# Kernel optimization log

Hardware: AMD Instinct MI355X
Metric: run time of the kernel (lower is better)

## Reference

```python
import jax, jax.numpy as jnp
import numpy as np

C_IN = 128      # pair channel
C_HID = 32      # per-head hidden dim
H = 4           # heads
INF = 1e9
LN_EPS = 1e-5


def setup_inputs() -> dict:
    key = jax.random.key(0)
    ks = jax.random.split(key, 8)
    B, N = 1, 256
    s = 0.02
    return {
        "x": jax.random.normal(ks[0], (B, N, N, C_IN), dtype=jnp.float32),
        "mask": jnp.ones((B, N, N), dtype=jnp.float32),
        "ln_w": jnp.ones((C_IN,), dtype=jnp.float32),
        "ln_b": jnp.zeros((C_IN,), dtype=jnp.float32),
        "w_b": jax.random.normal(ks[1], (H, C_IN), dtype=jnp.float32) * s,      # triangle-bias linear (no bias)
        "w_q": jax.random.normal(ks[2], (H * C_HID, C_IN), dtype=jnp.float32) * s,
        "w_k": jax.random.normal(ks[3], (H * C_HID, C_IN), dtype=jnp.float32) * s,
        "w_v": jax.random.normal(ks[4], (H * C_HID, C_IN), dtype=jnp.float32) * s,
        "w_g": jax.random.normal(ks[5], (H * C_HID, C_IN), dtype=jnp.float32) * s,
        "b_g": jnp.ones((H * C_HID,), dtype=jnp.float32),
        "w_o": jax.random.normal(ks[6], (C_IN, H * C_HID), dtype=jnp.float32) * s,
        "b_o": jnp.zeros((C_IN,), dtype=jnp.float32),
    }


def reference(x, mask, ln_w, ln_b, w_b, w_q, w_k, w_v, w_g, b_g, w_o, b_o):
    # starting=True -> no transpose
    # LayerNorm over channel dim
    mu = jnp.mean(x, axis=-1, keepdims=True)
    var = jnp.var(x, axis=-1, keepdims=True)
    xn = (x - mu) * jax.lax.rsqrt(var + LN_EPS) * ln_w + ln_b            # [B,I,J,C]

    # mask bias: [B, I, 1, 1, J]
    mask_bias = (INF * (mask - 1.0))[..., :, None, None, :]

    # triangle bias: linear -> [B,I,J,H] -> permute -> [B,H,I,J] -> [B,1,H,I,J]
    tri_bias = jnp.einsum("bijc,hc->bhij", xn, w_b)[:, None]

    # QKV projections, per-head: weights reshaped to [H, D, C]
    Wq = w_q.reshape(H, C_HID, C_IN)
    Wk = w_k.reshape(H, C_HID, C_IN)
    Wv = w_v.reshape(H, C_HID, C_IN)
    scale = 1.0 / np.sqrt(C_HID)
    q = jnp.einsum("bijc,hdc->bihjd", xn, Wq) * scale                    # [B,I,H,J,D]
    k = jnp.einsum("bijc,hdc->bihjd", xn, Wk)
    v = jnp.einsum("bijc,hdc->bihjd", xn, Wv)

    # attention over the J (column) axis of each row i
    a = jnp.einsum("bihqd,bihkd->bihqk", q, k) + mask_bias + tri_bias    # [B,I,H,J,J]
    a = jax.nn.softmax(a, axis=-1)
    o = jnp.einsum("bihqk,bihkd->biqhd", a, v)                           # [B,I,J,H,D]

    # sigmoid gating
    g = jax.nn.sigmoid(jnp.einsum("bijc,ec->bije", xn, w_g) + b_g)       # [B,I,J,H*D]
    o = o.reshape(*o.shape[:-2], H * C_HID) * g

    # output projection
    return jnp.einsum("bije,ce->bijc", o, w_o) + b_o                     # [B,I,J,C_in]
```

## Files before the change

kernel.cpp:

```cpp
#include <hip/hip_runtime.h>

#define N 256
#define C 128
#define H 4
#define D 32
#define NP (N*N)
#define LN_EPS 1e-5f
#define LOG2E 1.4426950408889634f

__device__ __forceinline__ void barrier_lgkm() {
    __asm__ volatile("s_waitcnt lgkmcnt(0)" ::: "memory");
    __builtin_amdgcn_sched_barrier(0);
    __builtin_amdgcn_s_barrier();
    __builtin_amdgcn_sched_barrier(0);
}

using f32x4 = __attribute__((ext_vector_type(4))) float;
using bf8   = __attribute__((ext_vector_type(8))) short;
using u16x4 = __attribute__((ext_vector_type(4))) unsigned short;

__device__ __forceinline__ float bf2f(ushort u) {
    union { uint u; float f; } v; v.u = ((uint)u) << 16; return v.f;
}
__device__ __forceinline__ ushort f2bf(float f) {
    union { float f; uint u; } v; v.f = f;
    uint u = v.u;
    u += 0x7fffu + ((u >> 16) & 1u);
    return (ushort)(u >> 16);
}
__device__ __forceinline__ ushort f2bf_trunc(float f) {
    union { float f; uint u; } v; v.f = f;
    return (ushort)(v.u >> 16);
}

__global__ __launch_bounds__(256) void prep_weights(
    const float* __restrict__ wq, const float* __restrict__ wk,
    const float* __restrict__ wv, const float* __restrict__ wg,
    const float* __restrict__ wb, const float* __restrict__ wo,
    ushort* __restrict__ Wcat, ushort* __restrict__ WbPad, ushort* __restrict__ Wo)
{
    int t = blockIdx.x * 256 + threadIdx.x;
    const float scale = 0.17677669529663689f * LOG2E;
    float v;
    if (t < 16384)       v = wq[t] * scale;
    else if (t < 32768)  v = wk[t - 16384];
    else if (t < 49152)  v = wv[t - 32768];
    else                 v = wg[t - 49152];
    Wcat[t] = f2bf(v);
    if (t < 16384) Wo[t] = f2bf(wo[t]);
    if (t < 2048)  WbPad[t] = (t < 512) ? f2bf(wb[t]) : (ushort)0;
}

__global__ __launch_bounds__(512, 4) void ln_proj(
    const float* __restrict__ x, const float* __restrict__ lnw,
    const float* __restrict__ lnb, const ushort* __restrict__ Wcat,
    const ushort* __restrict__ WbPad, const float* __restrict__ bg,
    ushort* __restrict__ qb, ushort* __restrict__ kb,
    ushort* __restrict__ vbT, ushort* __restrict__ gate,
    ushort* __restrict__ tri_p)
{
    __shared__ ushort At[64 * 128];
    int mt = blockIdx.x;
    int t  = threadIdx.x;
    int wave = t >> 6, lane = t & 63;
    int lane32 = lane & 31, rsel = lane >> 5;

    {
        const float4 w4 = ((const float4*)lnw)[lane32];
        const float4 b4 = ((const float4*)lnb)[lane32];
        const float* xb = x + (size_t)mt * 64 * C;
        float4 xv[4];
        #pragma unroll
        for (int pp = 0; pp < 4; pp++) {
            int r = pp * 16 + wave * 2 + rsel;
            xv[pp] = ((const float4*)(xb + r * C))[lane32];
        }
        #pragma unroll
        for (int pp = 0; pp < 4; pp++) {
            int r = pp * 16 + wave * 2 + rsel;
            float4 v = xv[pp];
            float s  = v.x + v.y + v.z + v.w;
            float ss = v.x*v.x + v.y*v.y + v.z*v.z + v.w*v.w;
            #pragma unroll
            for (int m = 1; m < 32; m <<= 1) {
                s  += __shfl_xor(s, m, 64);
                ss += __shfl_xor(ss, m, 64);
            }
            float mean = s * (1.f / 128.f);
            float var  = ss * (1.f / 128.f) - mean * mean;
            float rstd = rsqrtf(var + LN_EPS);
            u16x4 o;
            o[0] = f2bf((v.x - mean) * rstd * w4.x + b4.x);
            o[1] = f2bf((v.y - mean) * rstd * w4.y + b4.y);
            o[2] = f2bf((v.z - mean) * rstd * w4.z + b4.z);
            o[3] = f2bf((v.w - mean) * rstd * w4.w + b4.w);
            int c8 = lane32 >> 1;
            int chunk = r * 16 + (c8 ^ (r & 7));
            *(u16x4*)&At[chunk * 8 + (lane32 & 1) * 4] = o;
        }
    }
    barrier_lgkm();

    int lrow = lane & 15, quad = lane >> 4;
    int wr = wave >> 2, wc = wave & 3;

    bf8 afr[4][2];
    #pragma unroll
    for (int ks = 0; ks < 4; ks++) {
        int c8 = ks * 4 + quad;
        #pragma unroll
        for (int mi = 0; mi < 2; mi++) {
            int row = wr * 32 + mi * 16 + lrow;
            afr[ks][mi] = *(const bf8*)&At[(row * 16 + (c8 ^ (row & 7))) * 8];
        }
    }

    if (wc == 0) {
        f32x4 at0 = (f32x4){0.f,0.f,0.f,0.f}, at1 = (f32x4){0.f,0.f,0.f,0.f};
        #pragma unroll
        for (int ks = 0; ks < 4; ks++) {
            bf8 bt = *(const bf8*)(WbPad + lrow * C + (ks * 4 + quad) * 8);
            at0 = __builtin_amdgcn_mfma_f32_16x16x32_bf16(afr[ks][0], bt, at0, 0, 0, 0);
            at1 = __builtin_amdgcn_mfma_f32_16x16x32_bf16(afr[ks][1], bt, at1, 0, 0, 0);
        }
        if (lrow < 4) {
            int q = mt >> 2;
            int qc = q >> 4, quadq = (q >> 2) & 3, rr = q & 3;
            #pragma unroll
            for (int mi = 0; mi < 2; mi++) {
                #pragma unroll
                for (int r = 0; r < 4; r++) {
                    int k = (mt & 3) * 64 + wr * 32 + mi * 16 + quad * 4 + r;
                    int n = k >> 4, lk = k & 15;
                    int lanet = quadq * 16 + lk;
                    int v2 = n * 4 + rr, j = v2 >> 3, m2 = v2 & 7;
                    float val = (mi == 0) ? at0[r] : at1[r];
                    tri_p[lrow * 65536 + ((qc * 8 + j) * 64 + lanet) * 8 + m2] =
                        f2bf(val * LOG2E);
                }
            }
        }
    }

    #pragma unroll 1
    for (int nt = 0; nt < 4; nt++) {
        const ushort* Wt = Wcat + (size_t)nt * 128 * C;
        f32x4 acc[2][2];
        #pragma unroll
        for (int mi = 0; mi < 2; mi++)
            #pragma unroll
            for (int ni = 0; ni < 2; ni++) acc[mi][ni] = (f32x4){0.f, 0.f, 0.f, 0.f};

        #pragma unroll
        for (int ks = 0; ks < 4; ks++) {
            int c8 = ks * 4 + quad;
            bf8 b0 = *(const bf8*)(Wt + (size_t)(wc * 32 + lrow)      * C + c8 * 8);
            bf8 b1 = *(const bf8*)(Wt + (size_t)(wc * 32 + 16 + lrow) * C + c8 * 8);
            acc[0][0] = __builtin_amdgcn_mfma_f32_16x16x32_bf16(afr[ks][0], b0, acc[0][0], 0, 0, 0);
            acc[0][1] = __builtin_amdgcn_mfma_f32_16x16x32_bf16(afr[ks][0], b1, acc[0][1], 0, 0, 0);
            acc[1][0] = __builtin_amdgcn_mfma_f32_16x16x32_bf16(afr[ks][1], b0, acc[1][0], 0, 0, 0);
            acc[1][1] = __builtin_amdgcn_mfma_f32_16x16x32_bf16(afr[ks][1], b1, acc[1][1], 0, 0, 0);
        }

        barrier_lgkm();
        if (nt == 2) {
            #pragma unroll
            for (int mi = 0; mi < 2; mi++) {
                #pragma unroll
                for (int ni = 0; ni < 2; ni++) {
                    int col = wc * 32 + ni * 16 + lrow;
                    #pragma unroll
                    for (int r = 0; r < 4; r++) {
                        int keyl = wr * 32 + mi * 16 + quad * 4 + r;
                        At[col * 64 + (keyl ^ ((col & 7) << 3))] = f2bf(acc[mi][ni][r]);
                    }
                }
            }
            barrier_lgkm();
            int i_row = mt >> 2, kq = mt & 3;
            #pragma unroll
            for (int itr = 0; itr < 2; itr++) {
                int oidx = itr * 512 + t;
                int col = oidx >> 3, kc = oidx & 7;
                bf8 val = *(const bf8*)&At[col * 64 + ((kc * 8) ^ ((col & 7) << 3))];
                *(bf8*)&vbT[(size_t)(i_row * 128 + col) * N + kq * 64 + kc * 8] = val;
            }
        } else {
            ushort* dst = (nt == 0) ? qb : (nt == 1) ? kb : gate;
            float g0 = 0.f, g1 = 0.f;
            if (nt == 3) { g0 = bg[wc * 32 + lrow]; g1 = bg[wc * 32 + 16 + lrow]; }
            #pragma unroll
            for (int mi = 0; mi < 2; mi++) {
                #pragma unroll
                for (int ni = 0; ni < 2; ni++) {
                    int col = wc * 32 + ni * 16 + lrow;
                    #pragma unroll
                    for (int r = 0; r < 4; r++) {
                        int row = wr * 32 + mi * 16 + quad * 4 + r;
                        float vv = acc[mi][ni][r];
                        if (nt == 3)
                            vv = 1.f / (1.f + __expf(-(vv + ((ni == 0) ? g0 : g1))));
                        At[(row * 16 + ((col >> 3) ^ (row & 7))) * 8 + (col & 7)] = f2bf(vv);
                    }
                }
            }
            barrier_lgkm();
            #pragma unroll
            for (int itr = 0; itr < 2; itr++) {
                int oidx = itr * 512 + t;
                int row = oidx >> 4, c8 = oidx & 15;
                bf8 val = *(const bf8*)&At[(row * 16 + (c8 ^ (row & 7))) * 8];
                *(bf8*)&dst[(size_t)(mt * 64 + row) * C + c8 * 8] = val;
            }
        }
    }
}

__global__ __launch_bounds__(512, 4) void attn_out(
    const ushort* __restrict__ qb, const ushort* __restrict__ kb,
    const ushort* __restrict__ vbT, const ushort* __restrict__ tri_p,
    const float* __restrict__ mask, const ushort* __restrict__ gate,
    const ushort* __restrict__ Wo, const float* __restrict__ bo,
    float* __restrict__ out)
{
    __shared__ ushort Kf[8192];
    __shared__ ushort Vf[8192];
    __shared__ ushort Pf[8][2048];

    int i  = blockIdx.x;
    int qh = blockIdx.y;
    int t  = threadIdx.x;
    int wave = t >> 6, lane = t & 63;
    int lrow = lane & 15, quad = lane >> 4;
    int qc = qh * 8 + wave;

    float mb[16];
    #pragma unroll
    for (int n = 0; n < 16; n++)
        mb[n] = (1e9f * LOG2E) * (mask[i * N + n * 16 + lrow] - 1.0f);

    f32x4 oacc[8];
    #pragma unroll
    for (int ct = 0; ct < 8; ct++) oacc[ct] = (f32x4){0.f, 0.f, 0.f, 0.f};

    ushort* Pw = &Pf[wave][0];
    const int pq = quad * 32 + (lrow & 7);
    const int l3 = (lrow >> 3) & 1;

    #pragma unroll 1
    for (int h = 0; h < 4; h++) {
        bf8 aq = *(const bf8*)(qb + (size_t)(i * N + qc * 16 + lrow) * C
                               + h * D + quad * 8);
        barrier_lgkm();
        {
            const ushort* kt = kb + (size_t)(i * N) * C + h * D;
            #pragma unroll
            for (int it = 0; it < 2; it++) {
                int idx = it * 512 + t;
                int key = idx >> 2, d0 = (idx & 3) * 8;
                bf8 kv = *(const bf8*)(kt + (size_t)key * C + d0);
                int c = (idx >> 6) * 64 + (idx & 3) * 16 + ((idx >> 2) & 15);
                *(bf8*)&Kf[c * 8] = kv;
            }
        }
        {
            const ushort* vt = vbT + (size_t)((i * H + h) * D) * N;
            #pragma unroll
            for (int it = 0; it < 2; it++) {
                int idx = it * 512 + t;
                bf8 vv = *(const bf8*)(vt + idx * 8);
                int c = (idx >> 9) * 512 + ((idx >> 2) & 7) * 64 + (idx & 3) * 16 + ((idx >> 5) & 15);
                c ^= (c >> 6) & 7;
                *(bf8*)&Vf[c * 8] = vv;
            }
        }
        barrier_lgkm();

        float sum[4] = {0.f, 0.f, 0.f, 0.f};
        f32x4 o[2];
        o[0] = (f32x4){0.f, 0.f, 0.f, 0.f};
        o[1] = (f32x4){0.f, 0.f, 0.f, 0.f};
        const ushort* trih = tri_p + (size_t)h * 65536;

        #pragma unroll
        for (int half = 0; half < 2; half++) {
            const ushort* tp = trih + ((size_t)(qc * 8 + half * 4) * 64 + lane) * 8;
            #pragma unroll
            for (int p = 0; p < 4; p++) {
                bf8 tf = *(const bf8*)(tp + p * 512);
                #pragma unroll
                for (int j = 0; j < 2; j++) {
                    int n8 = p * 2 + j;
                    bf8 kf = *(const bf8*)&Kf[((half * 8 + n8) * 64 + lane) * 8];
                    f32x4 s = __builtin_amdgcn_mfma_f32_16x16x32_bf16(
                        aq, kf, (f32x4){0.f, 0.f, 0.f, 0.f}, 0, 0, 0);
                    int pa = (n8 >> 1) * 512 + (((n8 << 1) + l3) & 3) * 128 + pq;
                    #pragma unroll
                    for (int r = 0; r < 4; r++) {
                        float tb = bf2f(((const ushort*)&tf)[j * 4 + r]);
                        float e  = exp2f(s[r] + tb + mb[half * 8 + n8]);
                        sum[r]  += e;
                        Pw[pa + r * 8] = f2bf_trunc(e);
                    }
                }
            }
            __asm__ volatile("s_waitcnt lgkmcnt(0)" ::: "memory");
            __builtin_amdgcn_sched_barrier(0);

            __builtin_amdgcn_s_setprio(1);
            #pragma unroll
            for (int ks = 0; ks < 4; ks++) {
                bf8 ap = *(const bf8*)&Pw[(ks * 64 + lane) * 8];
                int ksg = half * 4 + ks;
                #pragma unroll
                for (int nv = 0; nv < 2; nv++) {
                    int c = nv * 512 + ksg * 64 + (lane ^ (ksg & 7));
                    bf8 bv = *(const bf8*)&Vf[c * 8];
                    o[nv] = __builtin_amdgcn_mfma_f32_16x16x32_bf16(ap, bv, o[nv], 0, 0, 0);
                }
            }
            __builtin_amdgcn_s_setprio(0);
        }

        #pragma unroll
        for (int r = 0; r < 4; r++) {
            float s = sum[r];
            s += __shfl_xor(s, 1, 64);
            s += __shfl_xor(s, 2, 64);
            s += __shfl_xor(s, 4, 64);
            s += __shfl_xor(s, 8, 64);
            sum[r] = 1.f / s;
        }
        const ushort* gt = gate + (size_t)(i * N + qc * 16) * C + h * D;
        #pragma unroll
        for (int nv = 0; nv < 2; nv++) {
            #pragma unroll
            for (int r = 0; r < 4; r++) {
                float g = bf2f(gt[(quad * 4 + r) * C + nv * 16 + lrow]);
                float val = o[nv][r] * sum[r] * g;
                Pw[(nv * 2 + l3) * 128 + pq + r * 8] = f2bf(val);
            }
        }
        __asm__ volatile("s_waitcnt lgkmcnt(0)" ::: "memory");
        __builtin_amdgcn_sched_barrier(0);

        bf8 ap = *(const bf8*)&Pw[lane * 8];
        __builtin_amdgcn_s_setprio(1);
        #pragma unroll
        for (int ct = 0; ct < 8; ct++) {
            bf8 wv = *(const bf8*)(Wo + (size_t)(ct * 16 + lrow) * 128 + h * D + quad * 8);
            oacc[ct] = __builtin_amdgcn_mfma_f32_16x16x32_bf16(ap, wv, oacc[ct], 0, 0, 0);
        }
        __builtin_amdgcn_s_setprio(0);
    }

    #pragma unroll
    for (int ct = 0; ct < 8; ct++) {
        float bias = bo[ct * 16 + lrow];
        #pragma unroll
        for (int r = 0; r < 4; r++) {
            int qg = qc * 16 + quad * 4 + r;
            out[(size_t)(i * N + qg) * C + ct * 16 + lrow] = oacc[ct][r] + bias;
        }
    }
}

extern "C" void kernel_launch(void* const* d_in, const int* in_sizes, int n_in,
                              void* d_out, int out_size, void* d_ws, size_t ws_size,
                              hipStream_t stream)
{
    const float* x    = (const float*)d_in[0];
    const float* mask = (const float*)d_in[1];
    const float* lnw  = (const float*)d_in[2];
    const float* lnb  = (const float*)d_in[3];
    const float* wb   = (const float*)d_in[4];
    const float* wq   = (const float*)d_in[5];
    const float* wk   = (const float*)d_in[6];
    const float* wv   = (const float*)d_in[7];
    const float* wg   = (const float*)d_in[8];
    const float* bg   = (const float*)d_in[9];
    const float* wo   = (const float*)d_in[10];
    const float* bo   = (const float*)d_in[11];
    float* out = (float*)d_out;

    uintptr_t w = (uintptr_t)d_ws;
    ushort* qb    = (ushort*)w; w += (size_t)NP * C * 2;
    ushort* kb    = (ushort*)w; w += (size_t)NP * C * 2;
    ushort* vbT   = (ushort*)w; w += (size_t)NP * C * 2;
    ushort* gate  = (ushort*)w; w += (size_t)NP * C * 2;
    ushort* tri_p = (ushort*)w; w += (size_t)H * NP * 2;
    ushort* Wcat  = (ushort*)w; w += 512 * 128 * 2;
    ushort* WbPad = (ushort*)w; w += 16 * 128 * 2;
    ushort* Wo    = (ushort*)w; w += 128 * 128 * 2;

    prep_weights<<<256, 256, 0, stream>>>(wq, wk, wv, wg, wb, wo, Wcat, WbPad, Wo);
    ln_proj<<<NP / 64, 512, 0, stream>>>(x, lnw, lnb, Wcat, WbPad, bg,
                                         qb, kb, vbT, gate, tri_p);
    attn_out<<<dim3(N, 2), 512, 0, stream>>>(qb, kb, vbT, tri_p, mask, gate,
                                             Wo, bo, out);
}
```

Baseline: 184.4 us.

## Fuse LN, QKVG projection and row attention into one per-row kernel

The q/k/v/gate projection now runs inside the attention kernel, one 1024-thread block per row i. LayerNorm output stays in LDS and K/V are built directly in shared memory, so the large bf16 q/k/vT/gate intermediates no longer round-trip through global memory. The triangle bias moves to a separate lightweight kernel that recomputes LayerNorm and does a scalar dot-product reduction, and the mask bias is staged in LDS. In exchange, x is read and normalised twice, LDS use per block is much larger, and there are only 256 blocks, which may limit occupancy and latency hiding.

New measurement: 227.6 us. 1.23x slower.

```diff
diff --git a/kernel.cpp b/kernel.cpp
--- a/kernel.cpp
+++ b/kernel.cpp
@@ -14,6 +14,10 @@
     __builtin_amdgcn_s_barrier();
     __builtin_amdgcn_sched_barrier(0);
 }
+__device__ __forceinline__ void drain_lds() {
+    __asm__ volatile("s_waitcnt lgkmcnt(0)" ::: "memory");
+    __builtin_amdgcn_sched_barrier(0);
+}
 
 using f32x4 = __attribute__((ext_vector_type(4))) float;
 using bf8   = __attribute__((ext_vector_type(8))) short;
@@ -36,8 +40,8 @@
 __global__ __launch_bounds__(256) void prep_weights(
     const float* __restrict__ wq, const float* __restrict__ wk,
     const float* __restrict__ wv, const float* __restrict__ wg,
-    const float* __restrict__ wb, const float* __restrict__ wo,
-    ushort* __restrict__ Wcat, ushort* __restrict__ WbPad, ushort* __restrict__ Wo)
+    const float* __restrict__ wo,
+    ushort* __restrict__ Wcat, ushort* __restrict__ Wo)
 {
     int t = blockIdx.x * 256 + threadIdx.x;
     const float scale = 0.17677669529663689f * LOG2E;
@@ -48,37 +52,94 @@
     else                 v = wg[t - 49152];
     Wcat[t] = f2bf(v);
     if (t < 16384) Wo[t] = f2bf(wo[t]);
-    if (t < 2048)  WbPad[t] = (t < 512) ? f2bf(wb[t]) : (ushort)0;
-}
-
-__global__ __launch_bounds__(512, 4) void ln_proj(
+}
+
+__global__ __launch_bounds__(256) void ln_tri(
+    const float* __restrict__ x, const float* __restrict__ lnw,
+    const float* __restrict__ lnb, const float* __restrict__ wb,
+    ushort* __restrict__ tri_p)
+{
+    int t = threadIdx.x;
+    int wave = t >> 6, lane = t & 63;
+    int lane32 = lane & 31, rsel = lane >> 5;
+    const float4 w4 = ((const float4*)lnw)[lane32];
+    const float4 b4 = ((const float4*)lnb)[lane32];
+    float4 wb0 = ((const float4*)(wb      ))[lane32];
+    float4 wb1 = ((const float4*)(wb + 128))[lane32];
+    float4 wb2 = ((const float4*)(wb + 256))[lane32];
+    float4 wb3 = ((const float4*)(wb + 384))[lane32];
+
+    #pragma unroll 1
+    for (int pp = 0; pp < 8; pp++) {
+        int p = blockIdx.x * 64 + pp * 8 + wave * 2 + rsel;
+        float4 v = ((const float4*)(x + (size_t)p * C))[lane32];
+        float s  = v.x + v.y + v.z + v.w;
+        float ss = v.x*v.x + v.y*v.y + v.z*v.z + v.w*v.w;
+        #pragma unroll
+        for (int m = 1; m < 32; m <<= 1) {
+            s  += __shfl_xor(s, m, 64);
+            ss += __shfl_xor(ss, m, 64);
+        }
+        float mean = s * (1.f / 128.f);
+        float var  = ss * (1.f / 128.f) - mean * mean;
+        float rstd = rsqrtf(var + LN_EPS);
+        float x0 = (v.x - mean) * rstd * w4.x + b4.x;
+        float x1 = (v.y - mean) * rstd * w4.y + b4.y;
+        float x2 = (v.z - mean) * rstd * w4.z + b4.z;
+        float x3 = (v.w - mean) * rstd * w4.w + b4.w;
+        float a0 = x0*wb0.x + x1*wb0.y + x2*wb0.z + x3*wb0.w;
+        float a1 = x0*wb1.x + x1*wb1.y + x2*wb1.z + x3*wb1.w;
+        float a2 = x0*wb2.x + x1*wb2.y + x2*wb2.z + x3*wb2.w;
+        float a3 = x0*wb3.x + x1*wb3.y + x2*wb3.z + x3*wb3.w;
+        #pragma unroll
+        for (int m = 1; m < 32; m <<= 1) {
+            a0 += __shfl_xor(a0, m, 64);
+            a1 += __shfl_xor(a1, m, 64);
+            a2 += __shfl_xor(a2, m, 64);
+            a3 += __shfl_xor(a3, m, 64);
+        }
+        if (lane32 < 4) {
+            float av = (lane32 == 0) ? a0 : (lane32 == 1) ? a1
+                     : (lane32 == 2) ? a2 : a3;
+            int q = p >> 8, k = p & 255;
+            int qc = q >> 4, quadq = (q >> 2) & 3, rr = q & 3;
+            int n = k >> 4, lk = k & 15;
+            int lanet = quadq * 16 + lk;
+            int v2 = n * 4 + rr, j = v2 >> 3, m2 = v2 & 7;
+            tri_p[lane32 * 65536 + ((qc * 8 + j) * 64 + lanet) * 8 + m2] =
+                f2bf(av * LOG2E);
+        }
+    }
+}
+
+__global__ __launch_bounds__(1024, 4) void row_fused(
     const float* __restrict__ x, const float* __restrict__ lnw,
     const float* __restrict__ lnb, const ushort* __restrict__ Wcat,
-    const ushort* __restrict__ WbPad, const float* __restrict__ bg,
-    ushort* __restrict__ qb, ushort* __restrict__ kb,
-    ushort* __restrict__ vbT, ushort* __restrict__ gate,
-    ushort* __restrict__ tri_p)
+    const float* __restrict__ bg, const ushort* __restrict__ tri_p,
+    const float* __restrict__ mask, const ushort* __restrict__ Wo,
+    const float* __restrict__ bo, float* __restrict__ out)
 {
-    __shared__ ushort At[64 * 128];
-    int mt = blockIdx.x;
-    int t  = threadIdx.x;
+    __shared__ ushort Xn[256 * 128];
+    __shared__ ushort Kf[8192];
+    __shared__ ushort Vf[8192];
+    __shared__ ushort Pf[16 * 1024];
+    __shared__ float  Ml[256];
+
+    int i = blockIdx.x;
+    int t = threadIdx.x;
     int wave = t >> 6, lane = t & 63;
     int lane32 = lane & 31, rsel = lane >> 5;
+    int lrow = lane & 15, quad = lane >> 4;
 
     {
         const float4 w4 = ((const float4*)lnw)[lane32];
         const float4 b4 = ((const float4*)lnb)[lane32];
-        const float* xb = x + (size_t)mt * 64 * C;
-        float4 xv[4];
-        #pragma unroll
-        for (int pp = 0; pp < 4; pp++) {
-            int r = pp * 16 + wave * 2 + rsel;
-            xv[pp] = ((const float4*)(xb + r * C))[lane32];
-        }
-        #pragma unroll
-        for (int pp = 0; pp < 4; pp++) {
-            int r = pp * 16 + wave * 2 + rsel;
-            float4 v = xv[pp];
+        const float* xb = x + (size_t)i * N * C;
+        if (t < 256) Ml[t] = (1e9f * LOG2E) * (mask[i * N + t] - 1.f);
+        #pragma unroll
+        for (int pp = 0; pp < 8; pp++) {
+            int r = pp * 32 + wave * 2 + rsel;
+            float4 v = ((const float4*)(xb + r * C))[lane32];
             float s  = v.x + v.y + v.z + v.w;
             float ss = v.x*v.x + v.y*v.y + v.z*v.z + v.w*v.w;
             #pragma unroll
@@ -96,232 +157,126 @@
             o[3] = f2bf((v.w - mean) * rstd * w4.w + b4.w);
             int c8 = lane32 >> 1;
             int chunk = r * 16 + (c8 ^ (r & 7));
-            *(u16x4*)&At[chunk * 8 + (lane32 & 1) * 4] = o;
+            *(u16x4*)&Xn[chunk * 8 + (lane32 & 1) * 4] = o;
         }
     }
     barrier_lgkm();
-
-    int lrow = lane & 15, quad = lane >> 4;
-    int wr = wave >> 2, wc = wave & 3;
-
-    bf8 afr[4][2];
-    #pragma unroll
-    for (int ks = 0; ks < 4; ks++) {
-        int c8 = ks * 4 + quad;
-        #pragma unroll
-        for (int mi = 0; mi < 2; mi++) {
-            int row = wr * 32 + mi * 16 + lrow;
-            afr[ks][mi] = *(const bf8*)&At[(row * 16 + (c8 ^ (row & 7))) * 8];
-        }
-    }
-
-    if (wc == 0) {
-        f32x4 at0 = (f32x4){0.f,0.f,0.f,0.f}, at1 = (f32x4){0.f,0.f,0.f,0.f};
-        #pragma unroll
-        for (int ks = 0; ks < 4; ks++) {
-            bf8 bt = *(const bf8*)(WbPad + lrow * C + (ks * 4 + quad) * 8);
-            at0 = __builtin_amdgcn_mfma_f32_16x16x32_bf16(afr[ks][0], bt, at0, 0, 0, 0);
-            at1 = __builtin_amdgcn_mfma_f32_16x16x32_bf16(afr[ks][1], bt, at1, 0, 0, 0);
-        }
-        if (lrow < 4) {
-            int q = mt >> 2;
-            int qc = q >> 4, quadq = (q >> 2) & 3, rr = q & 3;
-            #pragma unroll
-            for (int mi = 0; mi < 2; mi++) {
-                #pragma unroll
-                for (int r = 0; r < 4; r++) {
-                    int k = (mt & 3) * 64 + wr * 32 + mi * 16 + quad * 4 + r;
-                    int n = k >> 4, lk = k & 15;
-                    int lanet = quadq * 16 + lk;
-                    int v2 = n * 4 + rr, j = v2 >> 3, m2 = v2 & 7;
-                    float val = (mi == 0) ? at0[r] : at1[r];
-                    tri_p[lrow * 65536 + ((qc * 8 + j) * 64 + lanet) * 8 + m2] =
-                        f2bf(val * LOG2E);
-                }
-            }
-        }
-    }
-
-    #pragma unroll 1
-    for (int nt = 0; nt < 4; nt++) {
-        const ushort* Wt = Wcat + (size_t)nt * 128 * C;
-        f32x4 acc[2][2];
-        #pragma unroll
-        for (int mi = 0; mi < 2; mi++)
-            #pragma unroll
-            for (int ni = 0; ni < 2; ni++) acc[mi][ni] = (f32x4){0.f, 0.f, 0.f, 0.f};
-
-        #pragma unroll
-        for (int ks = 0; ks < 4; ks++) {
-            int c8 = ks * 4 + quad;
-            bf8 b0 = *(const bf8*)(Wt + (size_t)(wc * 32 + lrow)      * C + c8 * 8);
-            bf8 b1 = *(const bf8*)(Wt + (size_t)(wc * 32 + 16 + lrow) * C + c8 * 8);
-            acc[0][0] = __builtin_amdgcn_mfma_f32_16x16x32_bf16(afr[ks][0], b0, acc[0][0], 0, 0, 0);
-            acc[0][1] = __builtin_amdgcn_mfma_f32_16x16x32_bf16(afr[ks][0], b1, acc[0][1], 0, 0, 0);
-            acc[1][0] = __builtin_amdgcn_mfma_f32_16x16x32_bf16(afr[ks][1], b0, acc[1][0], 0, 0, 0);
-            acc[1][1] = __builtin_amdgcn_mfma_f32_16x16x32_bf16(afr[ks][1], b1, acc[1][1], 0, 0, 0);
-        }
-
-        barrier_lgkm();
-        if (nt == 2) {
-            #pragma unroll
-            for (int mi = 0; mi < 2; mi++) {
-                #pragma unroll
-                for (int ni = 0; ni < 2; ni++) {
-                    int col = wc * 32 + ni * 16 + lrow;
-                    #pragma unroll
-                    for (int r = 0; r < 4; r++) {
-                        int keyl = wr * 32 + mi * 16 + quad * 4 + r;
-                        At[col * 64 + (keyl ^ ((col & 7) << 3))] = f2bf(acc[mi][ni][r]);
-                    }
-                }
-            }
-            barrier_lgkm();
-            int i_row = mt >> 2, kq = mt & 3;
-            #pragma unroll
-            for (int itr = 0; itr < 2; itr++) {
-                int oidx = itr * 512 + t;
-                int col = oidx >> 3, kc = oidx & 7;
-                bf8 val = *(const bf8*)&At[col * 64 + ((kc * 8) ^ ((col & 7) << 3))];
-                *(bf8*)&vbT[(size_t)(i_row * 128 + col) * N + kq * 64 + kc * 8] = val;
-            }
-        } else {
-            ushort* dst = (nt == 0) ? qb : (nt == 1) ? kb : gate;
-            float g0 = 0.f, g1 = 0.f;
-            if (nt == 3) { g0 = bg[wc * 32 + lrow]; g1 = bg[wc * 32 + 16 + lrow]; }
-            #pragma unroll
-            for (int mi = 0; mi < 2; mi++) {
-                #pragma unroll
-                for (int ni = 0; ni < 2; ni++) {
-                    int col = wc * 32 + ni * 16 + lrow;
-                    #pragma unroll
-                    for (int r = 0; r < 4; r++) {
-                        int row = wr * 32 + mi * 16 + quad * 4 + r;
-                        float vv = acc[mi][ni][r];
-                        if (nt == 3)
-                            vv = 1.f / (1.f + __expf(-(vv + ((ni == 0) ? g0 : g1))));
-                        At[(row * 16 + ((col >> 3) ^ (row & 7))) * 8 + (col & 7)] = f2bf(vv);
-                    }
-                }
-            }
-            barrier_lgkm();
-            #pragma unroll
-            for (int itr = 0; itr < 2; itr++) {
-                int oidx = itr * 512 + t;
-                int row = oidx >> 4, c8 = oidx & 15;
-                bf8 val = *(const bf8*)&At[(row * 16 + (c8 ^ (row & 7))) * 8];
-                *(bf8*)&dst[(size_t)(mt * 64 + row) * C + c8 * 8] = val;
-            }
-        }
-    }
-}
-
-__global__ __launch_bounds__(512, 4) void attn_out(
-    const ushort* __restrict__ qb, const ushort* __restrict__ kb,
-    const ushort* __restrict__ vbT, const ushort* __restrict__ tri_p,
-    const float* __restrict__ mask, const ushort* __restrict__ gate,
-    const ushort* __restrict__ Wo, const float* __restrict__ bo,
-    float* __restrict__ out)
-{
-    __shared__ ushort Kf[8192];
-    __shared__ ushort Vf[8192];
-    __shared__ ushort Pf[8][2048];
-
-    int i  = blockIdx.x;
-    int qh = blockIdx.y;
-    int t  = threadIdx.x;
-    int wave = t >> 6, lane = t & 63;
-    int lrow = lane & 15, quad = lane >> 4;
-    int qc = qh * 8 + wave;
-
-    float mb[16];
-    #pragma unroll
-    for (int n = 0; n < 16; n++)
-        mb[n] = (1e9f * LOG2E) * (mask[i * N + n * 16 + lrow] - 1.0f);
 
     f32x4 oacc[8];
     #pragma unroll
     for (int ct = 0; ct < 8; ct++) oacc[ct] = (f32x4){0.f, 0.f, 0.f, 0.f};
 
-    ushort* Pw = &Pf[wave][0];
+    ushort* Pw = Pf + wave * 1024;
     const int pq = quad * 32 + (lrow & 7);
     const int l3 = (lrow >> 3) & 1;
 
     #pragma unroll 1
     for (int h = 0; h < 4; h++) {
-        bf8 aq = *(const bf8*)(qb + (size_t)(i * N + qc * 16 + lrow) * C
-                               + h * D + quad * 8);
+        bf8 afr[4];
+        #pragma unroll
+        for (int ks = 0; ks < 4; ks++) {
+            int row = wave * 16 + lrow;
+            afr[ks] = *(const bf8*)&Xn[(row * 16 + ((ks * 4 + quad) ^ (row & 7))) * 8];
+        }
+        f32x4 qa[2], ka[2], va[2], ga[2];
+        #pragma unroll
+        for (int ni = 0; ni < 2; ni++) {
+            qa[ni] = (f32x4){0.f,0.f,0.f,0.f}; ka[ni] = (f32x4){0.f,0.f,0.f,0.f};
+            va[ni] = (f32x4){0.f,0.f,0.f,0.f}; ga[ni] = (f32x4){0.f,0.f,0.f,0.f};
+        }
+        const ushort* Wq_ = Wcat + (size_t)(h * 32) * C;
+        const ushort* Wk_ = Wcat + (size_t)(128 + h * 32) * C;
+        const ushort* Wv_ = Wcat + (size_t)(256 + h * 32) * C;
+        const ushort* Wg_ = Wcat + (size_t)(384 + h * 32) * C;
+        #pragma unroll
+        for (int ks = 0; ks < 4; ks++) {
+            #pragma unroll
+            for (int ni = 0; ni < 2; ni++) {
+                size_t ro = (size_t)(ni * 16 + lrow) * C + (ks * 4 + quad) * 8;
+                qa[ni] = __builtin_amdgcn_mfma_f32_16x16x32_bf16(afr[ks], *(const bf8*)(Wq_ + ro), qa[ni], 0, 0, 0);
+                ka[ni] = __builtin_amdgcn_mfma_f32_16x16x32_bf16(afr[ks], *(const bf8*)(Wk_ + ro), ka[ni], 0, 0, 0);
+                va[ni] = __builtin_amdgcn_mfma_f32_16x16x32_bf16(afr[ks], *(const bf8*)(Wv_ + ro), va[ni], 0, 0, 0);
+                ga[ni] = __builtin_amdgcn_mfma_f32_16x16x32_bf16(afr[ks], *(const bf8*)(Wg_ + ro), ga[ni], 0, 0, 0);
+            }
+        }
         barrier_lgkm();
+
+        #pragma unroll
+        for (int ni = 0; ni < 2; ni++) {
+            int d = lrow + 16 * ni;
+            #pragma unroll
+            for (int r = 0; r < 4; r++) {
+                int key = wave * 16 + quad * 4 + r;
+                Kf[((key >> 4) * 64 + (d >> 3) * 16 + (key & 15)) * 8 + (d & 7)] =
+                    f2bf(ka[ni][r]);
+                Vf[((d >> 4) * 512 + (key >> 5) * 64 +
+                    ((((key >> 3) & 3) * 16 + (d & 15)) ^ ((key >> 5) & 7))) * 8 +
+                   (key & 7)] = f2bf(va[ni][r]);
+                Pw[((d >> 3) * 16 + quad * 4 + r) * 8 + (d & 7)] = f2bf(qa[ni][r]);
+            }
+        }
+        float gr[2][4];
         {
-            const ushort* kt = kb + (size_t)(i * N) * C + h * D;
-            #pragma unroll
-            for (int it = 0; it < 2; it++) {
-                int idx = it * 512 + t;
-                int key = idx >> 2, d0 = (idx & 3) * 8;
-                bf8 kv = *(const bf8*)(kt + (size_t)key * C + d0);
-                int c = (idx >> 6) * 64 + (idx & 3) * 16 + ((idx >> 2) & 15);
-                *(bf8*)&Kf[c * 8] = kv;
-            }
-        }
-        {
-            const ushort* vt = vbT + (size_t)((i * H + h) * D) * N;
-            #pragma unroll
-            for (int it = 0; it < 2; it++) {
-                int idx = it * 512 + t;
-                bf8 vv = *(const bf8*)(vt + idx * 8);
-                int c = (idx >> 9) * 512 + ((idx >> 2) & 7) * 64 + (idx & 3) * 16 + ((idx >> 5) & 15);
-                c ^= (c >> 6) & 7;
-                *(bf8*)&Vf[c * 8] = vv;
-            }
+            float gb0 = bg[h * 32 + lrow], gb1 = bg[h * 32 + 16 + lrow];
+            #pragma unroll
+            for (int ni = 0; ni < 2; ni++)
+                #pragma unroll
+                for (int r = 0; r < 4; r++)
+                    gr[ni][r] = 1.f / (1.f + __expf(-(ga[ni][r] + (ni ? gb1 : gb0))));
         }
         barrier_lgkm();
+        bf8 aq = *(const bf8*)&Pw[(quad * 16 + lrow) * 8];
 
         float sum[4] = {0.f, 0.f, 0.f, 0.f};
-        f32x4 o[2];
-        o[0] = (f32x4){0.f, 0.f, 0.f, 0.f};
-        o[1] = (f32x4){0.f, 0.f, 0.f, 0.f};
+        f32x4 o2[2];
+        o2[0] = (f32x4){0.f,0.f,0.f,0.f};
+        o2[1] = (f32x4){0.f,0.f,0.f,0.f};
         const ushort* trih = tri_p + (size_t)h * 65536;
 
         #pragma unroll
         for (int half = 0; half < 2; half++) {
-            const ushort* tp = trih + ((size_t)(qc * 8 + half * 4) * 64 + lane) * 8;
-            #pragma unroll
-            for (int p = 0; p < 4; p++) {
-                bf8 tf = *(const bf8*)(tp + p * 512);
+            const ushort* tp = trih + ((size_t)(wave * 8 + half * 4) * 64 + lane) * 8;
+            bf8 tf[4];
+            #pragma unroll
+            for (int jj = 0; jj < 4; jj++)
+                tf[jj] = *(const bf8*)(tp + jj * 512);
+            float mbh[8];
+            #pragma unroll
+            for (int j8 = 0; j8 < 8; j8++)
+                mbh[j8] = Ml[(half * 8 + j8) * 16 + lrow];
+
+            #pragma unroll
+            for (int qq = 0; qq < 2; qq++) {
                 #pragma unroll
-                for (int j = 0; j < 2; j++) {
-                    int n8 = p * 2 + j;
-                    bf8 kf = *(const bf8*)&Kf[((half * 8 + n8) * 64 + lane) * 8];
+                for (int j = 0; j < 4; j++) {
+                    int n8h = qq * 4 + j;
+                    bf8 kf = *(const bf8*)&Kf[((half * 8 + n8h) * 64 + lane) * 8];
                     f32x4 s = __builtin_amdgcn_mfma_f32_16x16x32_bf16(
-                        aq, kf, (f32x4){0.f, 0.f, 0.f, 0.f}, 0, 0, 0);
-                    int pa = (n8 >> 1) * 512 + (((n8 << 1) + l3) & 3) * 128 + pq;
+                        aq, kf, (f32x4){0.f,0.f,0.f,0.f}, 0, 0, 0);
+                    int pa = (j >> 1) * 512 + (((j << 1) + l3) & 3) * 128 + pq;
                     #pragma unroll
                     for (int r = 0; r < 4; r++) {
-                        float tb = bf2f(((const ushort*)&tf)[j * 4 + r]);
-                        float e  = exp2f(s[r] + tb + mb[half * 8 + n8]);
+                        float tb = bf2f(((const ushort*)&tf[n8h >> 1])[((n8h & 1) << 2) + r]);
+                        float e  = exp2f(s[r] + tb + mbh[n8h]);
                         sum[r]  += e;
                         Pw[pa + r * 8] = f2bf_trunc(e);
                     }
                 }
-            }
-            __asm__ volatile("s_waitcnt lgkmcnt(0)" ::: "memory");
-            __builtin_amdgcn_sched_barrier(0);
-
-            __builtin_amdgcn_s_setprio(1);
-            #pragma unroll
-            for (int ks = 0; ks < 4; ks++) {
-                bf8 ap = *(const bf8*)&Pw[(ks * 64 + lane) * 8];
-                int ksg = half * 4 + ks;
+                drain_lds();
+                __builtin_amdgcn_s_setprio(1);
                 #pragma unroll
-                for (int nv = 0; nv < 2; nv++) {
-                    int c = nv * 512 + ksg * 64 + (lane ^ (ksg & 7));
-                    bf8 bv = *(const bf8*)&Vf[c * 8];
-                    o[nv] = __builtin_amdgcn_mfma_f32_16x16x32_bf16(ap, bv, o[nv], 0, 0, 0);
+                for (int ksl = 0; ksl < 2; ksl++) {
+                    bf8 ap = *(const bf8*)&Pw[(ksl * 64 + lane) * 8];
+                    int ksg = half * 4 + qq * 2 + ksl;
+                    #pragma unroll
+                    for (int nv = 0; nv < 2; nv++) {
+                        bf8 bv = *(const bf8*)&Vf[(nv * 512 + ksg * 64 + (lane ^ (ksg & 7))) * 8];
+                        o2[nv] = __builtin_amdgcn_mfma_f32_16x16x32_bf16(ap, bv, o2[nv], 0, 0, 0);
+                    }
                 }
-            }
-            __builtin_amdgcn_s_setprio(0);
-        }
-
+                __builtin_amdgcn_s_setprio(0);
+            }
+        }
         #pragma unroll
         for (int r = 0; r < 4; r++) {
             float s = sum[r];
@@ -331,25 +286,20 @@
             s += __shfl_xor(s, 8, 64);
             sum[r] = 1.f / s;
         }
-        const ushort* gt = gate + (size_t)(i * N + qc * 16) * C + h * D;
-        #pragma unroll
-        for (int nv = 0; nv < 2; nv++) {
+        #pragma unroll
+        for (int nv = 0; nv < 2; nv++)
             #pragma unroll
             for (int r = 0; r < 4; r++) {
-                float g = bf2f(gt[(quad * 4 + r) * C + nv * 16 + lrow]);
-                float val = o[nv][r] * sum[r] * g;
+                float val = o2[nv][r] * sum[r] * gr[nv][r];
                 Pw[(nv * 2 + l3) * 128 + pq + r * 8] = f2bf(val);
             }
-        }
-        __asm__ volatile("s_waitcnt lgkmcnt(0)" ::: "memory");
-        __builtin_amdgcn_sched_barrier(0);
-
-        bf8 ap = *(const bf8*)&Pw[lane * 8];
+        drain_lds();
+        bf8 ap2 = *(const bf8*)&Pw[lane * 8];
         __builtin_amdgcn_s_setprio(1);
         #pragma unroll
         for (int ct = 0; ct < 8; ct++) {
-            bf8 wv = *(const bf8*)(Wo + (size_t)(ct * 16 + lrow) * 128 + h * D + quad * 8);
-            oacc[ct] = __builtin_amdgcn_mfma_f32_16x16x32_bf16(ap, wv, oacc[ct], 0, 0, 0);
+            bf8 wv = *(const bf8*)(Wo + (size_t)(ct * 16 + lrow) * 128 + h * 32 + quad * 8);
+            oacc[ct] = __builtin_amdgcn_mfma_f32_16x16x32_bf16(ap2, wv, oacc[ct], 0, 0, 0);
         }
         __builtin_amdgcn_s_setprio(0);
     }
@@ -359,7 +309,7 @@
         float bias = bo[ct * 16 + lrow];
         #pragma unroll
         for (int r = 0; r < 4; r++) {
-            int qg = qc * 16 + quad * 4 + r;
+            int qg = wave * 16 + quad * 4 + r;
             out[(size_t)(i * N + qg) * C + ct * 16 + lrow] = oacc[ct][r] + bias;
         }
     }
@@ -384,18 +334,12 @@
     float* out = (float*)d_out;
 
     uintptr_t w = (uintptr_t)d_ws;
-    ushort* qb    = (ushort*)w; w += (size_t)NP * C * 2;
-    ushort* kb    = (ushort*)w; w += (size_t)NP * C * 2;
-    ushort* vbT   = (ushort*)w; w += (size_t)NP * C * 2;
-    ushort* gate  = (ushort*)w; w += (size_t)NP * C * 2;
     ushort* tri_p = (ushort*)w; w += (size_t)H * NP * 2;
     ushort* Wcat  = (ushort*)w; w += 512 * 128 * 2;
-    ushort* WbPad = (ushort*)w; w += 16 * 128 * 2;
     ushort* Wo    = (ushort*)w; w += 128 * 128 * 2;
 
-    prep_weights<<<256, 256, 0, stream>>>(wq, wk, wv, wg, wb, wo, Wcat, WbPad, Wo);
-    ln_proj<<<NP / 64, 512, 0, stream>>>(x, lnw, lnb, Wcat, WbPad, bg,
-                                         qb, kb, vbT, gate, tri_p);
-    attn_out<<<dim3(N, 2), 512, 0, stream>>>(qb, kb, vbT, tri_p, mask, gate,
-                                             Wo, bo, out);
-}
+    prep_weights<<<256, 256, 0, stream>>>(wq, wk, wv, wg, wo, Wcat, Wo);
+    ln_tri<<<NP / 64, 256, 0, stream>>>(x, lnw, lnb, wb, tri_p);
+    row_fused<<<N, 1024, 0, stream>>>(x, lnw, lnb, Wcat, bg, tri_p,
+                                      mask, Wo, bo, out);
+}
```

## Restructure ln_proj to per-wave row tiles and prefetch next-head K/V in attention

Applied to the files above, without the earlier changes.

ln_proj now runs 256 threads per block, and each wave owns 16 rows across all 128 output columns. Each wave stages its own output in a private LDS slice, so the block-wide barriers become per-wave LDS drains, and V is written transposed straight from registers. In attn_out, the K, V and Q loads for the next head are issued into registers before the current head's compute, so global latency overlaps with the MFMA work. The cost is more registers per wave (8 accumulators plus the prefetch buffers), which could lower occupancy, and V is now written in narrower 8-byte stores.

Measured after the change: 229.5 us. 1.24x slower.

```diff
diff --git a/kernel.cpp b/kernel.cpp
--- a/kernel.cpp
+++ b/kernel.cpp
@@ -12,6 +12,10 @@
     __asm__ volatile("s_waitcnt lgkmcnt(0)" ::: "memory");
     __builtin_amdgcn_sched_barrier(0);
     __builtin_amdgcn_s_barrier();
+    __builtin_amdgcn_sched_barrier(0);
+}
+__device__ __forceinline__ void drain_lds() {
+    __asm__ volatile("s_waitcnt lgkmcnt(0)" ::: "memory");
     __builtin_amdgcn_sched_barrier(0);
 }
 
@@ -51,7 +55,7 @@
     if (t < 2048)  WbPad[t] = (t < 512) ? f2bf(wb[t]) : (ushort)0;
 }
 
-__global__ __launch_bounds__(512, 4) void ln_proj(
+__global__ __launch_bounds__(256, 4) void ln_proj(
     const float* __restrict__ x, const float* __restrict__ lnw,
     const float* __restrict__ lnb, const ushort* __restrict__ Wcat,
     const ushort* __restrict__ WbPad, const float* __restrict__ bg,
@@ -64,20 +68,21 @@
     int t  = threadIdx.x;
     int wave = t >> 6, lane = t & 63;
     int lane32 = lane & 31, rsel = lane >> 5;
+    int lrow = lane & 15, quad = lane >> 4;
 
     {
         const float4 w4 = ((const float4*)lnw)[lane32];
         const float4 b4 = ((const float4*)lnb)[lane32];
         const float* xb = x + (size_t)mt * 64 * C;
-        float4 xv[4];
-        #pragma unroll
-        for (int pp = 0; pp < 4; pp++) {
-            int r = pp * 16 + wave * 2 + rsel;
+        float4 xv[8];
+        #pragma unroll
+        for (int pp = 0; pp < 8; pp++) {
+            int r = wave * 16 + pp * 2 + rsel;
             xv[pp] = ((const float4*)(xb + r * C))[lane32];
         }
         #pragma unroll
-        for (int pp = 0; pp < 4; pp++) {
-            int r = pp * 16 + wave * 2 + rsel;
+        for (int pp = 0; pp < 8; pp++) {
+            int r = wave * 16 + pp * 2 + rsel;
             float4 v = xv[pp];
             float s  = v.x + v.y + v.z + v.w;
             float ss = v.x*v.x + v.y*v.y + v.z*v.z + v.w*v.w;
@@ -99,118 +104,87 @@
             *(u16x4*)&At[chunk * 8 + (lane32 & 1) * 4] = o;
         }
     }
-    barrier_lgkm();
-
-    int lrow = lane & 15, quad = lane >> 4;
-    int wr = wave >> 2, wc = wave & 3;
-
-    bf8 afr[4][2];
+    drain_lds();
+
+    bf8 afr[4];
     #pragma unroll
     for (int ks = 0; ks < 4; ks++) {
-        int c8 = ks * 4 + quad;
-        #pragma unroll
-        for (int mi = 0; mi < 2; mi++) {
-            int row = wr * 32 + mi * 16 + lrow;
-            afr[ks][mi] = *(const bf8*)&At[(row * 16 + (c8 ^ (row & 7))) * 8];
-        }
-    }
-
-    if (wc == 0) {
-        f32x4 at0 = (f32x4){0.f,0.f,0.f,0.f}, at1 = (f32x4){0.f,0.f,0.f,0.f};
+        int row = wave * 16 + lrow;
+        afr[ks] = *(const bf8*)&At[(row * 16 + ((ks * 4 + quad) ^ (row & 7))) * 8];
+    }
+    drain_lds();
+
+    {
+        f32x4 at = (f32x4){0.f, 0.f, 0.f, 0.f};
         #pragma unroll
         for (int ks = 0; ks < 4; ks++) {
             bf8 bt = *(const bf8*)(WbPad + lrow * C + (ks * 4 + quad) * 8);
-            at0 = __builtin_amdgcn_mfma_f32_16x16x32_bf16(afr[ks][0], bt, at0, 0, 0, 0);
-            at1 = __builtin_amdgcn_mfma_f32_16x16x32_bf16(afr[ks][1], bt, at1, 0, 0, 0);
+            at = __builtin_amdgcn_mfma_f32_16x16x32_bf16(afr[ks], bt, at, 0, 0, 0);
         }
         if (lrow < 4) {
             int q = mt >> 2;
             int qc = q >> 4, quadq = (q >> 2) & 3, rr = q & 3;
             #pragma unroll
-            for (int mi = 0; mi < 2; mi++) {
-                #pragma unroll
-                for (int r = 0; r < 4; r++) {
-                    int k = (mt & 3) * 64 + wr * 32 + mi * 16 + quad * 4 + r;
-                    int n = k >> 4, lk = k & 15;
-                    int lanet = quadq * 16 + lk;
-                    int v2 = n * 4 + rr, j = v2 >> 3, m2 = v2 & 7;
-                    float val = (mi == 0) ? at0[r] : at1[r];
-                    tri_p[lrow * 65536 + ((qc * 8 + j) * 64 + lanet) * 8 + m2] =
-                        f2bf(val * LOG2E);
-                }
-            }
-        }
-    }
-
+            for (int r = 0; r < 4; r++) {
+                int k = (mt & 3) * 64 + wave * 16 + quad * 4 + r;
+                int n = k >> 4, lk = k & 15;
+                int lanet = quadq * 16 + lk;
+                int v2 = n * 4 + rr, j = v2 >> 3, m2 = v2 & 7;
+                tri_p[lrow * 65536 + ((qc * 8 + j) * 64 + lanet) * 8 + m2] =
+                    f2bf(at[r] * LOG2E);
+            }
+        }
+    }
+
+    ushort* Sw = At + wave * 16 * 128;
     #pragma unroll 1
     for (int nt = 0; nt < 4; nt++) {
         const ushort* Wt = Wcat + (size_t)nt * 128 * C;
-        f32x4 acc[2][2];
-        #pragma unroll
-        for (int mi = 0; mi < 2; mi++)
-            #pragma unroll
-            for (int ni = 0; ni < 2; ni++) acc[mi][ni] = (f32x4){0.f, 0.f, 0.f, 0.f};
+        f32x4 acc[8];
+        #pragma unroll
+        for (int ni = 0; ni < 8; ni++) acc[ni] = (f32x4){0.f, 0.f, 0.f, 0.f};
 
         #pragma unroll
         for (int ks = 0; ks < 4; ks++) {
-            int c8 = ks * 4 + quad;
-            bf8 b0 = *(const bf8*)(Wt + (size_t)(wc * 32 + lrow)      * C + c8 * 8);
-            bf8 b1 = *(const bf8*)(Wt + (size_t)(wc * 32 + 16 + lrow) * C + c8 * 8);
-            acc[0][0] = __builtin_amdgcn_mfma_f32_16x16x32_bf16(afr[ks][0], b0, acc[0][0], 0, 0, 0);
-            acc[0][1] = __builtin_amdgcn_mfma_f32_16x16x32_bf16(afr[ks][0], b1, acc[0][1], 0, 0, 0);
-            acc[1][0] = __builtin_amdgcn_mfma_f32_16x16x32_bf16(afr[ks][1], b0, acc[1][0], 0, 0, 0);
-            acc[1][1] = __builtin_amdgcn_mfma_f32_16x16x32_bf16(afr[ks][1], b1, acc[1][1], 0, 0, 0);
-        }
-
-        barrier_lgkm();
+            #pragma unroll
+            for (int ni = 0; ni < 8; ni++) {
+                bf8 b = *(const bf8*)(Wt + (size_t)(ni * 16 + lrow) * C + (ks * 4 + quad) * 8);
+                acc[ni] = __builtin_amdgcn_mfma_f32_16x16x32_bf16(afr[ks], b, acc[ni], 0, 0, 0);
+            }
+        }
+
         if (nt == 2) {
-            #pragma unroll
-            for (int mi = 0; mi < 2; mi++) {
+            int i_row = mt >> 2;
+            int keyoff = (mt & 3) * 64 + wave * 16 + quad * 4;
+            #pragma unroll
+            for (int ni = 0; ni < 8; ni++) {
+                int col = ni * 16 + lrow;
+                union { ushort us[4]; uint2 u2; } pk;
                 #pragma unroll
-                for (int ni = 0; ni < 2; ni++) {
-                    int col = wc * 32 + ni * 16 + lrow;
-                    #pragma unroll
-                    for (int r = 0; r < 4; r++) {
-                        int keyl = wr * 32 + mi * 16 + quad * 4 + r;
-                        At[col * 64 + (keyl ^ ((col & 7) << 3))] = f2bf(acc[mi][ni][r]);
-                    }
-                }
-            }
-            barrier_lgkm();
-            int i_row = mt >> 2, kq = mt & 3;
-            #pragma unroll
-            for (int itr = 0; itr < 2; itr++) {
-                int oidx = itr * 512 + t;
-                int col = oidx >> 3, kc = oidx & 7;
-                bf8 val = *(const bf8*)&At[col * 64 + ((kc * 8) ^ ((col & 7) << 3))];
-                *(bf8*)&vbT[(size_t)(i_row * 128 + col) * N + kq * 64 + kc * 8] = val;
+                for (int r = 0; r < 4; r++) pk.us[r] = f2bf(acc[ni][r]);
+                *(uint2*)&vbT[(size_t)(i_row * 128 + col) * N + keyoff] = pk.u2;
             }
         } else {
             ushort* dst = (nt == 0) ? qb : (nt == 1) ? kb : gate;
-            float g0 = 0.f, g1 = 0.f;
-            if (nt == 3) { g0 = bg[wc * 32 + lrow]; g1 = bg[wc * 32 + 16 + lrow]; }
-            #pragma unroll
-            for (int mi = 0; mi < 2; mi++) {
+            #pragma unroll
+            for (int ni = 0; ni < 8; ni++) {
+                int col = ni * 16 + lrow;
+                float gb = (nt == 3) ? bg[col] : 0.f;
+                int colS = col ^ (quad << 3);
                 #pragma unroll
-                for (int ni = 0; ni < 2; ni++) {
-                    int col = wc * 32 + ni * 16 + lrow;
-                    #pragma unroll
-                    for (int r = 0; r < 4; r++) {
-                        int row = wr * 32 + mi * 16 + quad * 4 + r;
-                        float vv = acc[mi][ni][r];
-                        if (nt == 3)
-                            vv = 1.f / (1.f + __expf(-(vv + ((ni == 0) ? g0 : g1))));
-                        At[(row * 16 + ((col >> 3) ^ (row & 7))) * 8 + (col & 7)] = f2bf(vv);
-                    }
+                for (int r = 0; r < 4; r++) {
+                    float vv = acc[ni][r];
+                    if (nt == 3) vv = 1.f / (1.f + __expf(-(vv + gb)));
+                    Sw[(quad * 4 + r) * 128 + colS] = f2bf(vv);
                 }
             }
-            barrier_lgkm();
-            #pragma unroll
-            for (int itr = 0; itr < 2; itr++) {
-                int oidx = itr * 512 + t;
-                int row = oidx >> 4, c8 = oidx & 15;
-                bf8 val = *(const bf8*)&At[(row * 16 + (c8 ^ (row & 7))) * 8];
-                *(bf8*)&dst[(size_t)(mt * 64 + row) * C + c8 * 8] = val;
+            drain_lds();
+            #pragma unroll
+            for (int it = 0; it < 4; it++) {
+                int lin = it * 64 + lane;
+                int row = lin >> 4, c8 = lin & 15;
+                bf8 val = *(const bf8*)&Sw[row * 128 + (c8 ^ ((row >> 2) & 3)) * 8];
+                *(bf8*)&dst[(size_t)(mt * 64 + wave * 16 + row) * C + c8 * 8] = val;
             }
         }
     }
@@ -246,40 +220,46 @@
     ushort* Pw = &Pf[wave][0];
     const int pq = quad * 32 + (lrow & 7);
     const int l3 = (lrow >> 3) & 1;
+    const ushort* kt0 = kb + (size_t)(i * N) * C;
+    const ushort* vt0 = vbT + (size_t)(i * H * D) * N;
+
+    bf8 kpre[2], vpre[2], aq;
+    #pragma unroll
+    for (int it = 0; it < 2; it++) {
+        int idx = it * 512 + t;
+        kpre[it] = *(const bf8*)(kt0 + (size_t)(idx >> 2) * C + 0 * D + (idx & 3) * 8);
+        vpre[it] = *(const bf8*)(vt0 + (size_t)0 * D * N + idx * 8);
+    }
+    aq = *(const bf8*)(qb + (size_t)(i * N + qc * 16 + lrow) * C + 0 * D + quad * 8);
 
     #pragma unroll 1
     for (int h = 0; h < 4; h++) {
-        bf8 aq = *(const bf8*)(qb + (size_t)(i * N + qc * 16 + lrow) * C
-                               + h * D + quad * 8);
         barrier_lgkm();
-        {
-            const ushort* kt = kb + (size_t)(i * N) * C + h * D;
+        #pragma unroll
+        for (int it = 0; it < 2; it++) {
+            int idx = it * 512 + t;
+            int ck = (idx >> 6) * 64 + (idx & 3) * 16 + ((idx >> 2) & 15);
+            *(bf8*)&Kf[ck * 8] = kpre[it];
+            int cv = (idx >> 9) * 512 + ((idx >> 2) & 7) * 64 + (idx & 3) * 16 + ((idx >> 5) & 15);
+            cv ^= (cv >> 6) & 7;
+            *(bf8*)&Vf[cv * 8] = vpre[it];
+        }
+        bf8 aq_cur = aq;
+        if (h < 3) {
             #pragma unroll
             for (int it = 0; it < 2; it++) {
                 int idx = it * 512 + t;
-                int key = idx >> 2, d0 = (idx & 3) * 8;
-                bf8 kv = *(const bf8*)(kt + (size_t)key * C + d0);
-                int c = (idx >> 6) * 64 + (idx & 3) * 16 + ((idx >> 2) & 15);
-                *(bf8*)&Kf[c * 8] = kv;
-            }
-        }
-        {
-            const ushort* vt = vbT + (size_t)((i * H + h) * D) * N;
-            #pragma unroll
-            for (int it = 0; it < 2; it++) {
-                int idx = it * 512 + t;
-                bf8 vv = *(const bf8*)(vt + idx * 8);
-                int c = (idx >> 9) * 512 + ((idx >> 2) & 7) * 64 + (idx & 3) * 16 + ((idx >> 5) & 15);
-                c ^= (c >> 6) & 7;
-                *(bf8*)&Vf[c * 8] = vv;
-            }
+                kpre[it] = *(const bf8*)(kt0 + (size_t)(idx >> 2) * C + (h + 1) * D + (idx & 3) * 8);
+                vpre[it] = *(const bf8*)(vt0 + (size_t)(h + 1) * D * N + idx * 8);
+            }
+            aq = *(const bf8*)(qb + (size_t)(i * N + qc * 16 + lrow) * C + (h + 1) * D + quad * 8);
         }
         barrier_lgkm();
 
         float sum[4] = {0.f, 0.f, 0.f, 0.f};
-        f32x4 o[2];
-        o[0] = (f32x4){0.f, 0.f, 0.f, 0.f};
-        o[1] = (f32x4){0.f, 0.f, 0.f, 0.f};
+        f32x4 o2[2];
+        o2[0] = (f32x4){0.f, 0.f, 0.f, 0.f};
+        o2[1] = (f32x4){0.f, 0.f, 0.f, 0.f};
         const ushort* trih = tri_p + (size_t)h * 65536;
 
         #pragma unroll
@@ -293,7 +273,7 @@
                     int n8 = p * 2 + j;
                     bf8 kf = *(const bf8*)&Kf[((half * 8 + n8) * 64 + lane) * 8];
                     f32x4 s = __builtin_amdgcn_mfma_f32_16x16x32_bf16(
-                        aq, kf, (f32x4){0.f, 0.f, 0.f, 0.f}, 0, 0, 0);
+                        aq_cur, kf, (f32x4){0.f, 0.f, 0.f, 0.f}, 0, 0, 0);
                     int pa = (n8 >> 1) * 512 + (((n8 << 1) + l3) & 3) * 128 + pq;
                     #pragma unroll
                     for (int r = 0; r < 4; r++) {
@@ -304,8 +284,7 @@
                     }
                 }
             }
-            __asm__ volatile("s_waitcnt lgkmcnt(0)" ::: "memory");
-            __builtin_amdgcn_sched_barrier(0);
+            drain_lds();
 
             __builtin_amdgcn_s_setprio(1);
             #pragma unroll
@@ -316,7 +295,7 @@
                 for (int nv = 0; nv < 2; nv++) {
                     int c = nv * 512 + ksg * 64 + (lane ^ (ksg & 7));
                     bf8 bv = *(const bf8*)&Vf[c * 8];
-                    o[nv] = __builtin_amdgcn_mfma_f32_16x16x32_bf16(ap, bv, o[nv], 0, 0, 0);
+                    o2[nv] = __builtin_amdgcn_mfma_f32_16x16x32_bf16(ap, bv, o2[nv], 0, 0, 0);
                 }
             }
             __builtin_amdgcn_s_setprio(0);
@@ -337,19 +316,18 @@
             #pragma unroll
             for (int r = 0; r < 4; r++) {
                 float g = bf2f(gt[(quad * 4 + r) * C + nv * 16 + lrow]);
-                float val = o[nv][r] * sum[r] * g;
+                float val = o2[nv][r] * sum[r] * g;
                 Pw[(nv * 2 + l3) * 128 + pq + r * 8] = f2bf(val);
             }
         }
-        __asm__ volatile("s_waitcnt lgkmcnt(0)" ::: "memory");
-        __builtin_amdgcn_sched_barrier(0);
-
-        bf8 ap = *(const bf8*)&Pw[lane * 8];
+        drain_lds();
+
+        bf8 ap2 = *(const bf8*)&Pw[lane * 8];
         __builtin_amdgcn_s_setprio(1);
         #pragma unroll
         for (int ct = 0; ct < 8; ct++) {
             bf8 wv = *(const bf8*)(Wo + (size_t)(ct * 16 + lrow) * 128 + h * D + quad * 8);
-            oacc[ct] = __builtin_amdgcn_mfma_f32_16x16x32_bf16(ap, wv, oacc[ct], 0, 0, 0);
+            oacc[ct] = __builtin_amdgcn_mfma_f32_16x16x32_bf16(ap2, wv, oacc[ct], 0, 0, 0);
         }
         __builtin_amdgcn_s_setprio(0);
     }
@@ -394,7 +372,7 @@
     ushort* Wo    = (ushort*)w; w += 128 * 128 * 2;
 
     prep_weights<<<256, 256, 0, stream>>>(wq, wk, wv, wg, wb, wo, Wcat, WbPad, Wo);
-    ln_proj<<<NP / 64, 512, 0, stream>>>(x, lnw, lnb, Wcat, WbPad, bg,
+    ln_proj<<<NP / 64, 256, 0, stream>>>(x, lnw, lnb, Wcat, WbPad, bg,
                                          qb, kb, vbT, gate, tri_p);
     attn_out<<<dim3(N, 2), 512, 0, stream>>>(qb, kb, vbT, tri_p, mask, gate,
                                              Wo, bo, out);
```
